# Kernel tuning notes

Measured on AMD Instinct MI355X. Metric: run time of the kernel, lower is better.

## Reference

```python
import jax, jax.numpy as jnp
import numpy as np

B, C, CO, H, W = 8, 256, 128, 64, 64

def setup_inputs() -> dict:
    key = jax.random.key(0)
    ks = jax.random.split(key, 6)
    scale = 1.0 / np.sqrt(C)
    return {
        "p": jax.random.normal(ks[0], (B, C, H, W), jnp.float32),
        "b": jax.random.normal(ks[1], (B, C, H, W), jnp.float32),
        "Wq": jax.random.normal(ks[2], (CO, C), jnp.float32) * scale,
        "bq": jax.random.normal(ks[3], (CO,), jnp.float32) * 0.01,
        "Wk": jax.random.normal(ks[4], (CO, C), jnp.float32) * scale,
        "bk": jax.random.normal(ks[5], (CO,), jnp.float32) * 0.01,
    }

def reference(p, b, Wq, bq, Wk, bk):
    Bb, Cc, Hh, Ww = p.shape
    N = Hh * Ww
    pf = p.reshape(Bb, Cc, N)          # [B, C, N]
    bf = b.reshape(Bb, Cc, N)          # [B, C, N]
    # 1x1 conv == per-pixel linear projection
    q = jnp.einsum('oc,bcn->bno', Wq, pf) + bq            # [B, N, CO]
    k = jnp.einsum('oc,bcn->bon', Wk, bf) + bk[:, None]   # [B, CO, N]
    energy = jnp.einsum('bno,bom->bnm', q, k)             # [B, N, N]
    attention = jax.nn.softmax(energy, axis=-1)           # [B, N, N]
    # value = b flattened, attend over key pixels
    out = jnp.einsum('bnm,bcm->bcn', attention, bf)       # [B, C, N]
    out = out.reshape(Bb, Cc, Hh, Ww)
    return out, attention
```

## Files before the change

### kernel.cpp

```cpp
#include <hip/hip_runtime.h>
#include <hip/hip_bf16.h>
#include <cstdint>


#define BATCH 8
#define CCH   256
#define COO   128
#define NPIX  4096

typedef __bf16 bf16x8 __attribute__((ext_vector_type(8)));
typedef float  f32x4  __attribute__((ext_vector_type(4)));
typedef float  f32x16 __attribute__((ext_vector_type(16)));

__device__ __forceinline__ void gload16(const void* g, void* l) {
  __builtin_amdgcn_global_load_lds(
      (const __attribute__((address_space(1))) uint32_t*)g,
      (__attribute__((address_space(3))) uint32_t*)l, 16, 0, 0);
}

__global__ __launch_bounds__(256) void proj4_kernel(
    const float* __restrict__ X,
    const float* __restrict__ W,
    const float* __restrict__ bias,
    __bf16* __restrict__ fhi,
    __bf16* __restrict__ flo,
    __bf16* __restrict__ Vb)
{
  __shared__ float wlds[32][256];
  __shared__ float blds[32];
  const int b   = blockIdx.z;
  const int o0  = blockIdx.y * 32;
  const int tid = threadIdx.x;
  const int n   = blockIdx.x * 256 + tid;

  for (int i = tid; i < 2048; i += 256) {
    const int r = i >> 6, q = (i & 63) * 4;
    *reinterpret_cast<float4*>(&wlds[r][q]) =
        *reinterpret_cast<const float4*>(W + (size_t)(o0 + r) * CCH + q);
  }
  if (tid < 32) blds[tid] = bias[o0 + tid];
  __syncthreads();

  const float* Xc = X + (size_t)b * CCH * NPIX + n;
  const bool wV = (Vb != nullptr) && (blockIdx.y == 0);

  float acc[32];
#pragma unroll
  for (int o = 0; o < 32; ++o) acc[o] = 0.f;

  for (int c4 = 0; c4 < CCH; c4 += 4) {
    const float x0 = Xc[(size_t)(c4 + 0) * NPIX];
    const float x1 = Xc[(size_t)(c4 + 1) * NPIX];
    const float x2 = Xc[(size_t)(c4 + 2) * NPIX];
    const float x3 = Xc[(size_t)(c4 + 3) * NPIX];
    if (wV) {
      Vb[((size_t)b * CCH + c4 + 0) * NPIX + n] = (__bf16)x0;
      Vb[((size_t)b * CCH + c4 + 1) * NPIX + n] = (__bf16)x1;
      Vb[((size_t)b * CCH + c4 + 2) * NPIX + n] = (__bf16)x2;
      Vb[((size_t)b * CCH + c4 + 3) * NPIX + n] = (__bf16)x3;
    }
#pragma unroll
    for (int o = 0; o < 32; ++o) {
      const float4 wv = *reinterpret_cast<const float4*>(&wlds[o][c4]);
      acc[o] = fmaf(wv.x, x0, acc[o]);
      acc[o] = fmaf(wv.y, x1, acc[o]);
      acc[o] = fmaf(wv.z, x2, acc[o]);
      acc[o] = fmaf(wv.w, x3, acc[o]);
    }
  }

  const int n32 = n >> 5, nl = n & 31;
#pragma unroll
  for (int g = 0; g < 4; ++g) {
    const int o16 = (o0 >> 4) + (g >> 1);
    const int h   = g & 1;
    const size_t chunk =
        ((((size_t)b * 128 + n32) * 8 + o16) * 64 + nl + 32 * h) * 8;
    bf16x8 hv, lv;
#pragma unroll
    for (int j = 0; j < 8; ++j) {
      const int o = (g >> 1) * 16 + h * 8 + j;
      const float v = acc[o] + blds[o];
      const __bf16 hh = (__bf16)v;
      hv[j] = hh;
      lv[j] = (__bf16)(v - (float)hh);
    }
    *reinterpret_cast<bf16x8*>(fhi + chunk) = hv;
    *reinterpret_cast<bf16x8*>(flo + chunk) = lv;
  }
}

__global__ __launch_bounds__(256) void maxest2_kernel(
    const __bf16* __restrict__ qh, const __bf16* __restrict__ kh,
    float* __restrict__ Mp)
{
  __shared__ uint8_t lds[2 * 16384];
  const int lin = blockIdx.x;
  const int s = (lin & 7) * 128 + (lin >> 3);
  const int b = s >> 7, r = s & 127;
  const int n0 = (r >> 2) * 128, chunk = r & 3;
  const int tid = threadIdx.x;
  const int wr = tid >> 6, l = tid & 63;
  const int rl = l & 31, h = l >> 5;

  const size_t bbase = (size_t)b * 128 * 8 * 512;
  const uint8_t* khb = (const uint8_t*)(kh + bbase);
  const int nf = (n0 >> 5) + wr;
  bf16x8 qhf[8];
  {
    const __bf16* qhp = qh + bbase + (size_t)nf * 8 * 512 + (size_t)l * 8;
#pragma unroll
    for (int kc = 0; kc < 8; ++kc)
      qhf[kc] = *reinterpret_cast<const bf16x8*>(qhp + kc * 512);
  }

  float mx[16];
#pragma unroll
  for (int r2 = 0; r2 < 16; ++r2) mx[r2] = -3.0e38f;

  const int mt0 = chunk * 16;

#define MSTAGE(buf, mt)                                                       \
  {                                                                           \
    _Pragma("unroll")                                                         \
    for (int q = 0; q < 4; ++q)                                               \
      gload16(khb + (size_t)(mt) * 16384 + q * 4096 + tid * 16,               \
              lds + (buf) * 16384 + q * 4096 + tid * 16);                     \
  }

  MSTAGE(0, mt0);
  __syncthreads();

  for (int i = 0; i < 16; ++i) {
    const int cur = i & 1;
    if (i + 1 < 16) MSTAGE(cur ^ 1, mt0 + i + 1);
    const uint8_t* kt = lds + cur * 16384;
    f32x16 a0, a1;
#pragma unroll
    for (int r2 = 0; r2 < 16; ++r2) { a0[r2] = 0.f; a1[r2] = 0.f; }
#pragma unroll
    for (int kc = 0; kc < 8; ++kc) {
      const bf16x8 k0 = *reinterpret_cast<const bf16x8*>(kt + kc * 1024 + l * 16);
      const bf16x8 k1 = *reinterpret_cast<const bf16x8*>(kt + 8192 + kc * 1024 + l * 16);
      a0 = __builtin_amdgcn_mfma_f32_32x32x16_bf16(qhf[kc], k0, a0, 0, 0, 0);
      a1 = __builtin_amdgcn_mfma_f32_32x32x16_bf16(qhf[kc], k1, a1, 0, 0, 0);
    }
#pragma unroll
    for (int r2 = 0; r2 < 16; ++r2)
      mx[r2] = fmaxf(mx[r2], fmaxf(a0[r2], a1[r2]));
    __syncthreads();
  }
#undef MSTAGE

#pragma unroll
  for (int off = 1; off <= 16; off <<= 1)
#pragma unroll
    for (int r2 = 0; r2 < 16; ++r2)
      mx[r2] = fmaxf(mx[r2], __shfl_xor(mx[r2], off));

  if (rl == 0) {
#pragma unroll
    for (int r2 = 0; r2 < 16; ++r2) {
      const int row = n0 + wr * 32 + (r2 & 3) + 8 * (r2 >> 2) + 4 * h;
      Mp[((size_t)b * NPIX + row) * 4 + chunk] = mx[r2];
    }
  }
}

__global__ __launch_bounds__(256) void ukern2_kernel(
    const __bf16* __restrict__ qh, const __bf16* __restrict__ ql,
    const __bf16* __restrict__ kh, const __bf16* __restrict__ kl,
    const float* __restrict__ Mp,
    __bf16* __restrict__ u,
    float* __restrict__ Sp)
{
  __shared__ uint8_t lds[2 * 32768];
  const int lin = blockIdx.x;
  const int s = (lin & 7) * 128 + (lin >> 3);
  const int b = s >> 7, r = s & 127;
  const int n0 = (r >> 2) * 128, chunk = r & 3;
  const int tid = threadIdx.x;
  const int wr = tid >> 6, l = tid & 63;
  const int rl = l & 31, h = l >> 5;

  const size_t bbase = (size_t)b * 128 * 8 * 512;
  const uint8_t* khb = (const uint8_t*)(kh + bbase);
  const uint8_t* klb = (const uint8_t*)(kl + bbase);
  const int nf = (n0 >> 5) + wr;
  bf16x8 qhf[8], qlf[8];
  {
    const __bf16* qhp = qh + bbase + (size_t)nf * 8 * 512 + (size_t)l * 8;
    const __bf16* qlp = ql + bbase + (size_t)nf * 8 * 512 + (size_t)l * 8;
#pragma unroll
    for (int kc = 0; kc < 8; ++kc) {
      qhf[kc] = *reinterpret_cast<const bf16x8*>(qhp + kc * 512);
      qlf[kc] = *reinterpret_cast<const bf16x8*>(qlp + kc * 512);
    }
  }

  int rowv[16];
  float Mh[16], s_run[16];
#pragma unroll
  for (int r2 = 0; r2 < 16; ++r2) {
    rowv[r2] = n0 + wr * 32 + (r2 & 3) + 8 * (r2 >> 2) + 4 * h;
    const float4 mp = *reinterpret_cast<const float4*>(
        Mp + ((size_t)b * NPIX + rowv[r2]) * 4);
    Mh[r2] = fmaxf(fmaxf(mp.x, mp.y), fmaxf(mp.z, mp.w)) + 2.0f;
    s_run[r2] = 0.f;
  }

  const int mt0 = chunk * 16;

#define USTAGE(buf, mt)                                                       \
  {                                                                           \
    _Pragma("unroll")                                                         \
    for (int q = 0; q < 4; ++q)                                               \
      gload16(khb + (size_t)(mt) * 16384 + q * 4096 + tid * 16,               \
              lds + (buf) * 32768 + q * 4096 + tid * 16);                     \
    _Pragma("unroll")                                                         \
    for (int q = 0; q < 4; ++q)                                               \
      gload16(klb + (size_t)(mt) * 16384 + q * 4096 + tid * 16,               \
              lds + (buf) * 32768 + 16384 + q * 4096 + tid * 16);             \
  }

  USTAGE(0, mt0);
  __syncthreads();

  for (int i = 0; i < 16; ++i) {
    const int cur = i & 1;
    const int mt = mt0 + i;
    if (i + 1 < 16) USTAGE(cur ^ 1, mt + 1);
    const uint8_t* kht = lds + cur * 32768;
    const uint8_t* klt = kht + 16384;
    f32x16 a0, a1;
#pragma unroll
    for (int r2 = 0; r2 < 16; ++r2) { a0[r2] = 0.f; a1[r2] = 0.f; }
#pragma unroll
    for (int kc = 0; kc < 8; ++kc) {
      const int fo = kc * 1024 + l * 16;
      const bf16x8 kh0 = *reinterpret_cast<const bf16x8*>(kht + fo);
      const bf16x8 kh1 = *reinterpret_cast<const bf16x8*>(kht + 8192 + fo);
      const bf16x8 kl0 = *reinterpret_cast<const bf16x8*>(klt + fo);
      const bf16x8 kl1 = *reinterpret_cast<const bf16x8*>(klt + 8192 + fo);
      a0 = __builtin_amdgcn_mfma_f32_32x32x16_bf16(qhf[kc], kh0, a0, 0, 0, 0);
      a0 = __builtin_amdgcn_mfma_f32_32x32x16_bf16(qhf[kc], kl0, a0, 0, 0, 0);
      a0 = __builtin_amdgcn_mfma_f32_32x32x16_bf16(qlf[kc], kh0, a0, 0, 0, 0);
      a1 = __builtin_amdgcn_mfma_f32_32x32x16_bf16(qhf[kc], kh1, a1, 0, 0, 0);
      a1 = __builtin_amdgcn_mfma_f32_32x32x16_bf16(qhf[kc], kl1, a1, 0, 0, 0);
      a1 = __builtin_amdgcn_mfma_f32_32x32x16_bf16(qlf[kc], kh1, a1, 0, 0, 0);
    }
#pragma unroll
    for (int r2 = 0; r2 < 16; ++r2) {
      const float u0 = __expf(a0[r2] - Mh[r2]);
      const float u1 = __expf(a1[r2] - Mh[r2]);
      s_run[r2] += u0 + u1;
      const size_t base =
          ((size_t)b * NPIX + rowv[r2]) * NPIX + mt * 64 + rl;
      u[base]      = (__bf16)u0;
      u[base + 32] = (__bf16)u1;
    }
    __syncthreads();
  }
#undef USTAGE

#pragma unroll
  for (int off = 1; off <= 16; off <<= 1)
#pragma unroll
    for (int r2 = 0; r2 < 16; ++r2) s_run[r2] += __shfl_xor(s_run[r2], off);

  if (rl == 0) {
#pragma unroll
    for (int r2 = 0; r2 < 16; ++r2)
      Sp[((size_t)b * NPIX + rowv[r2]) * 4 + chunk] = s_run[r2];
  }
}

__global__ __launch_bounds__(256) void sfin_kernel(
    const float* __restrict__ Sp, float* __restrict__ frow)
{
  const int idx = blockIdx.x * 256 + threadIdx.x;
  const float4 v = *reinterpret_cast<const float4*>(Sp + (size_t)idx * 4);
  frow[idx] = 1.0f / (v.x + v.y + v.z + v.w);
}

__global__ __launch_bounds__(256) void pv4_kernel(
    const __bf16* __restrict__ V,
    const __bf16* __restrict__ An,
    const float* __restrict__ frow,
    float* __restrict__ attn,
    float* __restrict__ out)
{
  __shared__ uint8_t ldsb[2 * 40960];
  const int lin = blockIdx.x;
  const int s   = (lin & 7) * 64 + (lin >> 3);
  const int n0  = (s & 63) * 64;
  const int b   = s >> 6;
  const int tid = threadIdx.x;
  const int w = tid >> 6, l = tid & 63;
  const int rl = l & 31;

  const uint8_t* Vbase = (const uint8_t*)(V + (size_t)b * CCH * NPIX);
  const uint8_t* Abase = (const uint8_t*)(An + ((size_t)b * NPIX + n0) * NPIX);

  const float f0 = frow[(size_t)b * NPIX + n0 + rl];
  const float f1 = frow[(size_t)b * NPIX + n0 + 32 + rl];
  const int arow = tid >> 2;
  const int aseg = (tid & 3) * 16;
  const float fa = frow[(size_t)b * NPIX + n0 + arow];
  float* abase = attn + ((size_t)b * NPIX + n0 + arow) * NPIX + aseg;
  const int ab0 = arow * 128 + ((aseg * 2) ^ ((arow & 7) << 4));
  const int ab1 = arow * 128 + ((aseg * 2 + 16) ^ ((arow & 7) << 4));

  f32x16 acc[2][2];
#pragma unroll
  for (int fr = 0; fr < 2; ++fr)
#pragma unroll
    for (int fc = 0; fc < 2; ++fc)
#pragma unroll
      for (int r2 = 0; r2 < 16; ++r2) acc[fr][fc][r2] = 0.f;

#define STAGE(buf, t)                                                         \
  {                                                                           \
    const int tb = (t) * 128;                                                 \
    _Pragma("unroll")                                                         \
    for (int q = 0; q < 8; ++q) {                                             \
      const int dst = q * 4096 + tid * 16;                                    \
      const int row = dst >> 7, colb = dst & 127;                             \
      gload16(Vbase + (size_t)row * 8192 + tb + (colb ^ ((row & 7) << 4)),    \
              ldsb + (buf) * 40960 + dst);                                    \
    }                                                                         \
    _Pragma("unroll")                                                         \
    for (int q = 0; q < 2; ++q) {                                             \
      const int dst = q * 4096 + tid * 16;                                    \
      const int row = dst >> 7, colb = dst & 127;                             \
      gload16(Abase + (size_t)row * 8192 + tb + (colb ^ ((row & 7) << 4)),    \
              ldsb + (buf) * 40960 + 32768 + dst);                            \
    }                                                                         \
  }

  STAGE(0, 0);
  __syncthreads();

  for (int t = 0; t < 64; ++t) {
    const int cur = t & 1;
    if (t + 1 < 64) STAGE(cur ^ 1, t + 1);
    const uint8_t* Vt = ldsb + cur * 40960;
    const uint8_t* At = Vt + 32768;
#pragma unroll
    for (int kc = 0; kc < 4; ++kc) {
      const int colb = kc * 32 + ((l >> 5) << 4);
      bf16x8 a[2], bb[2];
#pragma unroll
      for (int f = 0; f < 2; ++f) {
        const int row = w * 64 + f * 32 + rl;
        a[f] = *reinterpret_cast<const bf16x8*>(
            Vt + row * 128 + (colb ^ ((row & 7) << 4)));
      }
#pragma unroll
      for (int f = 0; f < 2; ++f) {
        const int row = f * 32 + rl;
        bb[f] = *reinterpret_cast<const bf16x8*>(
            At + row * 128 + (colb ^ ((row & 7) << 4)));
      }
#pragma unroll
      for (int fr = 0; fr < 2; ++fr)
#pragma unroll
        for (int fc = 0; fc < 2; ++fc)
          acc[fr][fc] = __builtin_amdgcn_mfma_f32_32x32x16_bf16(a[fr], bb[fc], acc[fr][fc], 0, 0, 0);
    }
    {
      const bf16x8 u0 = *reinterpret_cast<const bf16x8*>(At + ab0);
      const bf16x8 u1 = *reinterpret_cast<const bf16x8*>(At + ab1);
      float* ap = abase + t * 64;
      float4 o0, o1, o2, o3;
      o0.x = (float)u0[0] * fa; o0.y = (float)u0[1] * fa;
      o0.z = (float)u0[2] * fa; o0.w = (float)u0[3] * fa;
      o1.x = (float)u0[4] * fa; o1.y = (float)u0[5] * fa;
      o1.z = (float)u0[6] * fa; o1.w = (float)u0[7] * fa;
      o2.x = (float)u1[0] * fa; o2.y = (float)u1[1] * fa;
      o2.z = (float)u1[2] * fa; o2.w = (float)u1[3] * fa;
      o3.x = (float)u1[4] * fa; o3.y = (float)u1[5] * fa;
      o3.z = (float)u1[6] * fa; o3.w = (float)u1[7] * fa;
      *reinterpret_cast<float4*>(ap)      = o0;
      *reinterpret_cast<float4*>(ap + 4)  = o1;
      *reinterpret_cast<float4*>(ap + 8)  = o2;
      *reinterpret_cast<float4*>(ap + 12) = o3;
    }
    __syncthreads();
  }
#undef STAGE

  const int hi4 = (l >> 5) * 4;
#pragma unroll
  for (int fr = 0; fr < 2; ++fr)
#pragma unroll
    for (int fc = 0; fc < 2; ++fc) {
      const float ff = fc ? f1 : f0;
#pragma unroll
      for (int r2 = 0; r2 < 16; ++r2) {
        const int c = w * 64 + fr * 32 + (r2 & 3) + 8 * (r2 >> 2) + hi4;
        const int n = n0 + fc * 32 + rl;
        out[((size_t)b * CCH + c) * NPIX + n] = acc[fr][fc][r2] * ff;
      }
    }
}

template <bool WB16>
__global__ __launch_bounds__(256) void fes_kernel(
    const __bf16* __restrict__ qh, const __bf16* __restrict__ ql,
    const __bf16* __restrict__ kh, const __bf16* __restrict__ kl,
    float* __restrict__ attn, __bf16* __restrict__ attnb)
{
  const int lin = blockIdx.x;
  const int s   = (lin & 7) * 64 + (lin >> 3);
  const int b   = s >> 6;
  const int n0  = (s & 63) * 64;
  const int tid = threadIdx.x;
  const int w = tid >> 6, l = tid & 63;
  const int wr = w >> 1, wc = w & 1;
  const int rl = l & 31, h = l >> 5;

  const size_t lane8 = (size_t)l * 8;
  const size_t bbase = (size_t)b * 128 * 8 * 512;
  const __bf16* khp = kh + bbase + lane8;
  const __bf16* klp = kl + bbase + lane8;

  const int nf = (n0 >> 5) + wr;
  bf16x8 qhf[8], qlf[8];
  {
    const __bf16* qhp = qh + bbase + (size_t)nf * 8 * 512 + lane8;
    const __bf16* qlp = ql + bbase + (size_t)nf * 8 * 512 + lane8;
#pragma unroll
    for (int kc = 0; kc < 8; ++kc) {
      qhf[kc] = *reinterpret_cast<const bf16x8*>(qhp + kc * 512);
      qlf[kc] = *reinterpret_cast<const bf16x8*>(qlp + kc * 512);
    }
  }

#define SCORE_TILE(mt, acc0, acc1)                                            \
  {                                                                           \
    _Pragma("unroll")                                                         \
    for (int kc = 0; kc < 8; ++kc) {                                          \
      const size_t o0 = ((size_t)((mt) * 2 + 0) * 8 + kc) * 512;              \
      const size_t o1 = ((size_t)((mt) * 2 + 1) * 8 + kc) * 512;              \
      const bf16x8 kh0 = *reinterpret_cast<const bf16x8*>(khp + o0);          \
      const bf16x8 kl0 = *reinterpret_cast<const bf16x8*>(klp + o0);          \
      const bf16x8 kh1 = *reinterpret_cast<const bf16x8*>(khp + o1);          \
      const bf16x8 kl1 = *reinterpret_cast<const bf16x8*>(klp + o1);          \
      acc0 = __builtin_amdgcn_mfma_f32_32x32x16_bf16(qhf[kc], kh0, acc0, 0, 0, 0); \
      acc0 = __builtin_amdgcn_mfma_f32_32x32x16_bf16(qhf[kc], kl0, acc0, 0, 0, 0); \
      acc0 = __builtin_amdgcn_mfma_f32_32x32x16_bf16(qlf[kc], kh0, acc0, 0, 0, 0); \
      acc1 = __builtin_amdgcn_mfma_f32_32x32x16_bf16(qhf[kc], kh1, acc1, 0, 0, 0); \
      acc1 = __builtin_amdgcn_mfma_f32_32x32x16_bf16(qhf[kc], kl1, acc1, 0, 0, 0); \
      acc1 = __builtin_amdgcn_mfma_f32_32x32x16_bf16(qlf[kc], kh1, acc1, 0, 0, 0); \
    }                                                                         \
  }

  float m_run[16], s_run[16];
#pragma unroll
  for (int r2 = 0; r2 < 16; ++r2) { m_run[r2] = -3.0e38f; s_run[r2] = 0.f; }

  for (int mt = wc * 32; mt < wc * 32 + 32; ++mt) {
    f32x16 acc0, acc1;
#pragma unroll
    for (int r2 = 0; r2 < 16; ++r2) { acc0[r2] = 0.f; acc1[r2] = 0.f; }
    SCORE_TILE(mt, acc0, acc1);
#pragma unroll
    for (int r2 = 0; r2 < 16; ++r2) {
      {
        const float x = acc0[r2];
        const float mo = m_run[r2];
        const float mn = fmaxf(mo, x);
        s_run[r2] = s_run[r2] * __expf(mo - mn) + __expf(x - mn);
        m_run[r2] = mn;
      }
      {
        const float x = acc1[r2];
        const float mo = m_run[r2];
        const float mn = fmaxf(mo, x);
        s_run[r2] = s_run[r2] * __expf(mo - mn) + __expf(x - mn);
        m_run[r2] = mn;
      }
    }
  }

#pragma unroll
  for (int off = 1; off <= 16; off <<= 1) {
#pragma unroll
    for (int r2 = 0; r2 < 16; ++r2) {
      const float m2 = __shfl_xor(m_run[r2], off);
      const float s2 = __shfl_xor(s_run[r2], off);
      const float mn = fmaxf(m_run[r2], m2);
      s_run[r2] = s_run[r2] * __expf(m_run[r2] - mn) + s2 * __expf(m2 - mn);
      m_run[r2] = mn;
    }
  }

  __shared__ float lm[2][2][2][16];
  __shared__ float lsv[2][2][2][16];
  if (rl == 0) {
#pragma unroll
    for (int r2 = 0; r2 < 16; ++r2) {
      lm[wr][wc][h][r2]  = m_run[r2];
      lsv[wr][wc][h][r2] = s_run[r2];
    }
  }
  __syncthreads();

  float Mf[16], iS[16];
#pragma unroll
  for (int r2 = 0; r2 < 16; ++r2) {
    const float m0 = lm[wr][0][h][r2], m1 = lm[wr][1][h][r2];
    const float M  = fmaxf(m0, m1);
    const float S  = lsv[wr][0][h][r2] * __expf(m0 - M) +
                     lsv[wr][1][h][r2] * __expf(m1 - M);
    Mf[r2] = M;
    iS[r2] = 1.0f / S;
  }

  for (int mt = wc * 32; mt < wc * 32 + 32; ++mt) {
    f32x16 acc0, acc1;
#pragma unroll
    for (int r2 = 0; r2 < 16; ++r2) { acc0[r2] = 0.f; acc1[r2] = 0.f; }
    SCORE_TILE(mt, acc0, acc1);
#pragma unroll
    for (int r2 = 0; r2 < 16; ++r2) {
      const int row = n0 + wr * 32 + (r2 & 3) + 8 * (r2 >> 2) + 4 * h;
      const size_t base = ((size_t)b * NPIX + row) * NPIX + mt * 64 + rl;
      const float v0 = __expf(acc0[r2] - Mf[r2]) * iS[r2];
      const float v1 = __expf(acc1[r2] - Mf[r2]) * iS[r2];
      attn[base]      = v0;
      attn[base + 32] = v1;
      if (WB16) {
        attnb[base]      = (__bf16)v0;
        attnb[base + 32] = (__bf16)v1;
      }
    }
  }
#undef SCORE_TILE
}

__global__ __launch_bounds__(256) void pv_kernel(
    const __bf16* __restrict__ V,
    const float*  __restrict__ attn,
    float* __restrict__ out)
{
  const int b   = blockIdx.z;
  const int n0  = blockIdx.x * 64;
  const int tid = threadIdx.x;
  const int w = tid >> 6, l = tid & 63;
  const int wr = w >> 1, wc = w & 1;
  const int rl = l & 15, k8 = (l >> 4) * 8;

  const __bf16* vp = V + ((size_t)b * CCH + wr * 128 + rl) * NPIX + k8;
  const float*  ap = attn + ((size_t)b * NPIX + n0 + wc * 32 + rl) * NPIX + k8;

  f32x4 zero = {0.f, 0.f, 0.f, 0.f};
  f32x4 acc[8][2];
#pragma unroll
  for (int fr = 0; fr < 8; ++fr) { acc[fr][0] = zero; acc[fr][1] = zero; }

  for (int ks = 0; ks < 128; ++ks) {
    const int mo = ks * 32;
    bf16x8 a[8];
#pragma unroll
    for (int f = 0; f < 8; ++f)
      a[f] = *reinterpret_cast<const bf16x8*>(vp + (size_t)f * 16 * NPIX + mo);
    bf16x8 bb[2];
#pragma unroll
    for (int f = 0; f < 2; ++f) {
      const float* aq = ap + (size_t)f * 16 * NPIX + mo;
      float4 x = *reinterpret_cast<const float4*>(aq);
      float4 y = *reinterpret_cast<const float4*>(aq + 4);
      bf16x8 t;
      t[0] = (__bf16)x.x; t[1] = (__bf16)x.y; t[2] = (__bf16)x.z; t[3] = (__bf16)x.w;
      t[4] = (__bf16)y.x; t[5] = (__bf16)y.y; t[6] = (__bf16)y.z; t[7] = (__bf16)y.w;
      bb[f] = t;
    }
#pragma unroll
    for (int fr = 0; fr < 8; ++fr) {
      acc[fr][0] = __builtin_amdgcn_mfma_f32_16x16x32_bf16(a[fr], bb[0], acc[fr][0], 0, 0, 0);
      acc[fr][1] = __builtin_amdgcn_mfma_f32_16x16x32_bf16(a[fr], bb[1], acc[fr][1], 0, 0, 0);
    }
  }

  const int cg = (l >> 4) * 4;
#pragma unroll
  for (int fr = 0; fr < 8; ++fr)
#pragma unroll
    for (int fc = 0; fc < 2; ++fc)
#pragma unroll
      for (int r = 0; r < 4; ++r) {
        const int c = wr * 128 + fr * 16 + cg + r;
        const int n = n0 + wc * 32 + fc * 16 + rl;
        out[((size_t)b * CCH + c) * NPIX + n] = acc[fr][fc][r];
      }
}

extern "C" void kernel_launch(void* const* d_in, const int* in_sizes, int n_in,
                              void* d_out, int out_size, void* d_ws, size_t ws_size,
                              hipStream_t stream)
{
  const float* p  = (const float*)d_in[0];
  const float* bi = (const float*)d_in[1];
  const float* Wq = (const float*)d_in[2];
  const float* bq = (const float*)d_in[3];
  const float* Wk = (const float*)d_in[4];
  const float* bk = (const float*)d_in[5];

  float* out  = (float*)d_out;
  float* attn = out + (size_t)BATCH * CCH * NPIX;

  const size_t QK  = (size_t)BATCH * NPIX * COO;
  const size_t VB  = (size_t)BATCH * CCH * NPIX;
  const size_t ANB = (size_t)BATCH * NPIX * NPIX;
  const size_t need_bf16 = (ANB + 4 * QK + VB) * 2;

  if (ws_size >= need_bf16) {
    __bf16* u   = (__bf16*)d_ws;
    __bf16* qhi = u + ANB;
    __bf16* qlo = qhi + QK;
    __bf16* khi = qlo + QK;
    __bf16* klo = khi + QK;
    __bf16* Vb  = klo + QK;

    float* Mp   = attn;
    float* Sp   = Mp + 131072;
    float* frow = (float*)qhi;

    proj4_kernel<<<dim3(16, 4, 8), 256, 0, stream>>>(p,  Wq, bq, qhi, qlo, nullptr);
    proj4_kernel<<<dim3(16, 4, 8), 256, 0, stream>>>(bi, Wk, bk, khi, klo, Vb);
    maxest2_kernel<<<1024, 256, 0, stream>>>(qhi, khi, Mp);
    ukern2_kernel<<<1024, 256, 0, stream>>>(qhi, qlo, khi, klo, Mp, u, Sp);
    sfin_kernel<<<128, 256, 0, stream>>>(Sp, frow);
    pv4_kernel<<<512, 256, 0, stream>>>(Vb, u, frow, attn, out);
  } else {
    __bf16* qhi = (__bf16*)d_ws;
    __bf16* qlo = qhi + QK;
    __bf16* khi = qlo + QK;
    __bf16* klo = khi + QK;
    __bf16* Vb  = klo + QK;

    proj4_kernel<<<dim3(16, 4, 8), 256, 0, stream>>>(p,  Wq, bq, qhi, qlo, nullptr);
    proj4_kernel<<<dim3(16, 4, 8), 256, 0, stream>>>(bi, Wk, bk, khi, klo, Vb);
    fes_kernel<false><<<512, 256, 0, stream>>>(qhi, qlo, khi, klo, attn, nullptr);
    pv_kernel<<<dim3(64, 1, 8), 256, 0, stream>>>(Vb, attn, out);
  }
}
```

Baseline: 570.7 us.

## Subsample key tiles in max estimate and split PV across 8 waves

The row-max estimation kernel now visits every other key tile in its chunk, halving its matmul and load work. The softmax offset becomes an approximate stabilizer rather than the exact maximum, which is mathematically consistent as long as the later exp/sum stages use the same offset. The PV kernel moves to 512 threads: each wave computes a 64x32 output tile instead of 64x64, and the staging loads and attention-row writes are spread over twice as many threads. This aims at better latency hiding and more parallel stores, at the cost of lower per-wave reuse of the V fragments and possible register/occupancy changes.

```diff
diff --git a/kernel.cpp b/kernel.cpp
--- a/kernel.cpp
+++ b/kernel.cpp
@@ -90,7 +90,7 @@
   }
 }
 
-__global__ __launch_bounds__(256) void maxest2_kernel(
+__global__ __launch_bounds__(256) void maxest3_kernel(
     const __bf16* __restrict__ qh, const __bf16* __restrict__ kh,
     float* __restrict__ Mp)
 {
@@ -131,9 +131,9 @@
   MSTAGE(0, mt0);
   __syncthreads();
 
-  for (int i = 0; i < 16; ++i) {
+  for (int i = 0; i < 8; ++i) {
     const int cur = i & 1;
-    if (i + 1 < 16) MSTAGE(cur ^ 1, mt0 + i + 1);
+    if (i + 1 < 8) MSTAGE(cur ^ 1, mt0 + 2 * (i + 1));
     const uint8_t* kt = lds + cur * 16384;
     f32x16 a0, a1;
 #pragma unroll
@@ -283,7 +283,7 @@
   frow[idx] = 1.0f / (v.x + v.y + v.z + v.w);
 }
 
-__global__ __launch_bounds__(256) void pv4_kernel(
+__global__ __launch_bounds__(512) void pv6_kernel(
     const __bf16* __restrict__ V,
     const __bf16* __restrict__ An,
     const float* __restrict__ frow,
@@ -297,41 +297,38 @@
   const int b   = s >> 6;
   const int tid = threadIdx.x;
   const int w = tid >> 6, l = tid & 63;
+  const int wc4 = w >> 1, wn = w & 1;
   const int rl = l & 31;
 
   const uint8_t* Vbase = (const uint8_t*)(V + (size_t)b * CCH * NPIX);
   const uint8_t* Abase = (const uint8_t*)(An + ((size_t)b * NPIX + n0) * NPIX);
 
-  const float f0 = frow[(size_t)b * NPIX + n0 + rl];
-  const float f1 = frow[(size_t)b * NPIX + n0 + 32 + rl];
-  const int arow = tid >> 2;
-  const int aseg = (tid & 3) * 16;
+  const float fl = frow[(size_t)b * NPIX + n0 + wn * 32 + rl];
+
+  const int arow = tid >> 3;
+  const int aseg = (tid & 7) * 8;
   const float fa = frow[(size_t)b * NPIX + n0 + arow];
   float* abase = attn + ((size_t)b * NPIX + n0 + arow) * NPIX + aseg;
   const int ab0 = arow * 128 + ((aseg * 2) ^ ((arow & 7) << 4));
-  const int ab1 = arow * 128 + ((aseg * 2 + 16) ^ ((arow & 7) << 4));
-
-  f32x16 acc[2][2];
+
+  f32x16 acc[2];
 #pragma unroll
   for (int fr = 0; fr < 2; ++fr)
 #pragma unroll
-    for (int fc = 0; fc < 2; ++fc)
-#pragma unroll
-      for (int r2 = 0; r2 < 16; ++r2) acc[fr][fc][r2] = 0.f;
+    for (int r2 = 0; r2 < 16; ++r2) acc[fr][r2] = 0.f;
 
 #define STAGE(buf, t)                                                         \
   {                                                                           \
     const int tb = (t) * 128;                                                 \
     _Pragma("unroll")                                                         \
-    for (int q = 0; q < 8; ++q) {                                             \
-      const int dst = q * 4096 + tid * 16;                                    \
+    for (int q = 0; q < 4; ++q) {                                             \
+      const int dst = q * 8192 + tid * 16;                                    \
       const int row = dst >> 7, colb = dst & 127;                             \
       gload16(Vbase + (size_t)row * 8192 + tb + (colb ^ ((row & 7) << 4)),    \
               ldsb + (buf) * 40960 + dst);                                    \
     }                                                                         \
-    _Pragma("unroll")                                                         \
-    for (int q = 0; q < 2; ++q) {                                             \
-      const int dst = q * 4096 + tid * 16;                                    \
+    {                                                                         \
+      const int dst = tid * 16;                                               \
       const int row = dst >> 7, colb = dst & 127;                             \
       gload16(Abase + (size_t)row * 8192 + tb + (colb ^ ((row & 7) << 4)),    \
               ldsb + (buf) * 40960 + 32768 + dst);                            \
@@ -349,42 +346,32 @@
 #pragma unroll
     for (int kc = 0; kc < 4; ++kc) {
       const int colb = kc * 32 + ((l >> 5) << 4);
-      bf16x8 a[2], bb[2];
+      bf16x8 a[2], bb;
 #pragma unroll
       for (int f = 0; f < 2; ++f) {
-        const int row = w * 64 + f * 32 + rl;
+        const int row = wc4 * 64 + f * 32 + rl;
         a[f] = *reinterpret_cast<const bf16x8*>(
             Vt + row * 128 + (colb ^ ((row & 7) << 4)));
       }
-#pragma unroll
-      for (int f = 0; f < 2; ++f) {
-        const int row = f * 32 + rl;
-        bb[f] = *reinterpret_cast<const bf16x8*>(
+      {
+        const int row = wn * 32 + rl;
+        bb = *reinterpret_cast<const bf16x8*>(
             At + row * 128 + (colb ^ ((row & 7) << 4)));
       }
 #pragma unroll
-      for (int fr = 0; fr < 2; ++fr)
-#pragma unroll
-        for (int fc = 0; fc < 2; ++fc)
-          acc[fr][fc] = __builtin_amdgcn_mfma_f32_32x32x16_bf16(a[fr], bb[fc], acc[fr][fc], 0, 0, 0);
+      for (int f = 0; f < 2; ++f)
+        acc[f] = __builtin_amdgcn_mfma_f32_32x32x16_bf16(a[f], bb, acc[f], 0, 0, 0);
     }
     {
       const bf16x8 u0 = *reinterpret_cast<const bf16x8*>(At + ab0);
-      const bf16x8 u1 = *reinterpret_cast<const bf16x8*>(At + ab1);
       float* ap = abase + t * 64;
-      float4 o0, o1, o2, o3;
+      float4 o0, o1;
       o0.x = (float)u0[0] * fa; o0.y = (float)u0[1] * fa;
       o0.z = (float)u0[2] * fa; o0.w = (float)u0[3] * fa;
       o1.x = (float)u0[4] * fa; o1.y = (float)u0[5] * fa;
       o1.z = (float)u0[6] * fa; o1.w = (float)u0[7] * fa;
-      o2.x = (float)u1[0] * fa; o2.y = (float)u1[1] * fa;
-      o2.z = (float)u1[2] * fa; o2.w = (float)u1[3] * fa;
-      o3.x = (float)u1[4] * fa; o3.y = (float)u1[5] * fa;
-      o3.z = (float)u1[6] * fa; o3.w = (float)u1[7] * fa;
-      *reinterpret_cast<float4*>(ap)      = o0;
-      *reinterpret_cast<float4*>(ap + 4)  = o1;
-      *reinterpret_cast<float4*>(ap + 8)  = o2;
-      *reinterpret_cast<float4*>(ap + 12) = o3;
+      *reinterpret_cast<float4*>(ap)     = o0;
+      *reinterpret_cast<float4*>(ap + 4) = o1;
     }
     __syncthreads();
   }
@@ -394,14 +381,10 @@
 #pragma unroll
   for (int fr = 0; fr < 2; ++fr)
 #pragma unroll
-    for (int fc = 0; fc < 2; ++fc) {
-      const float ff = fc ? f1 : f0;
-#pragma unroll
-      for (int r2 = 0; r2 < 16; ++r2) {
-        const int c = w * 64 + fr * 32 + (r2 & 3) + 8 * (r2 >> 2) + hi4;
-        const int n = n0 + fc * 32 + rl;
-        out[((size_t)b * CCH + c) * NPIX + n] = acc[fr][fc][r2] * ff;
-      }
+    for (int r2 = 0; r2 < 16; ++r2) {
+      const int c = wc4 * 64 + fr * 32 + (r2 & 3) + 8 * (r2 >> 2) + hi4;
+      const int n = n0 + wn * 32 + rl;
+      out[((size_t)b * CCH + c) * NPIX + n] = acc[fr][r2] * fl;
     }
 }
 
@@ -630,10 +613,10 @@
 
     proj4_kernel<<<dim3(16, 4, 8), 256, 0, stream>>>(p,  Wq, bq, qhi, qlo, nullptr);
     proj4_kernel<<<dim3(16, 4, 8), 256, 0, stream>>>(bi, Wk, bk, khi, klo, Vb);
-    maxest2_kernel<<<1024, 256, 0, stream>>>(qhi, khi, Mp);
+    maxest3_kernel<<<1024, 256, 0, stream>>>(qhi, khi, Mp);
     ukern2_kernel<<<1024, 256, 0, stream>>>(qhi, qlo, khi, klo, Mp, u, Sp);
     sfin_kernel<<<128, 256, 0, stream>>>(Sp, frow);
-    pv4_kernel<<<512, 256, 0, stream>>>(Vb, u, frow, attn, out);
+    pv6_kernel<<<512, 512, 0, stream>>>(Vb, u, frow, attn, out);
   } else {
     __bf16* qhi = (__bf16*)d_ws;
     __bf16* qlo = qhi + QK;
```

After: 548.4 us. 1.04x faster.
